# Optimization experiments

Hardware: AMD Instinct MI355X
Metric: run time of the kernel (lower is better)

## Reference

```python
import jax, jax.numpy as jnp
import numpy as np

B, N, F_, CI, C, CO = 2, 1024, 2048, 3, 80, 128
NB = 15          # DirResNet blocks
Q = C // 4


def _graph_bn(x, g, b, eps=1e-5):
    # BatchNorm over channels with stats over (batch, nodes) -- training-mode batch stats
    mu = jnp.mean(x, axis=(0, 1), keepdims=True)
    var = jnp.var(x, axis=(0, 1), keepdims=True)
    return (x - mu) * jax.lax.rsqrt(var + eps) * g + b


def _graph_conv(L, x, W0, W1, bias):
    # GraphConv with k=1: linear on [x, L @ x]
    return x @ W0 + jnp.einsum('bnm,bmc->bnc', L, x) @ W1 + bias


def _forward(inputs, L, Di, DiA, mask,
             conv1_W0, conv1_W1, conv1_b,
             rn_bn0_g, rn_bn0_b, rn_fc0_W, rn_fc0_b,
             rn_bn1_g, rn_bn1_b, rn_fc1_W, rn_fc1_b,
             bn1_g, bn1_b, bn2_g, bn2_b, bn3_g, bn3_b,
             conv2_W0, conv2_W1, conv2_b):
    v = _graph_conv(L, inputs, conv1_W0, conv1_W1, conv1_b)      # [B,N,C]
    f = jnp.zeros((B, F_, C), v.dtype)
    z = jnp.zeros_like(v)
    carry = (f, f, v, z, z)  # [f, tmp_f, v, tmp_v, tmp_v]

    def block(carry, p):
        f, tmp_f, v, tv0, tv1 = carry
        g0, b0, W0, c0, g1, b1, W1, c1 = p
        # Dirac: vertices -> faces (quaternion reshape: [B,N,C] -> [B,4N,C/4])
        Dv = jnp.matmul(Di, v.reshape(B, 4 * N, Q)).reshape(B, F_, C)
        x = jnp.concatenate([f, Dv], axis=-1)                    # [B,F,2C]
        f_new = jax.nn.elu(_graph_bn(x, g0, b0) @ W0 + c0) + tmp_f
        # Adjoint Dirac: faces -> vertices
        Df = jnp.matmul(DiA, f_new.reshape(B, 4 * F_, Q)).reshape(B, N, C)
        y = jnp.concatenate([v, Df], axis=-1)                    # [B,N,2C]
        v_new = jax.nn.elu(_graph_bn(y, g1, b1) @ W1 + c1) + tv0
        return (f_new, f, v_new, v, tv0), None

    carry, _ = jax.lax.scan(
        block, carry,
        (rn_bn0_g, rn_bn0_b, rn_fc0_W, rn_fc0_b,
         rn_bn1_g, rn_bn1_b, rn_fc1_W, rn_fc1_b))
    _, _, v2, v1, v0 = carry
    v = jax.nn.elu(_graph_bn(v2, bn1_g, bn1_b)
                   + _graph_bn(v1, bn2_g, bn2_b)
                   + _graph_bn(v0, bn3_g, bn3_b))
    # Dropout2d: identity (eval mode / deterministic reference)
    v = _graph_conv(L, v, conv2_W0, conv2_W1, conv2_b)           # [B,N,CO]
    out = (v * mask).sum(axis=1) / mask.sum(axis=1)              # masked mean pool -> [B,CO]
    return out


def setup_inputs() -> dict:
    key = jax.random.key(0)
    ks = jax.random.split(key, 32)
    s = 0.05
    d = {
        'inputs': jax.random.normal(ks[0], (B, N, CI), jnp.float32),
        'L': jax.random.normal(ks[1], (B, N, N), jnp.float32) / np.float32(np.sqrt(N)),
        'Di': jax.random.normal(ks[2], (B, 4 * F_, 4 * N), jnp.float32) / np.float32(np.sqrt(4 * N)),
        'DiA': jax.random.normal(ks[3], (B, 4 * N, 4 * F_), jnp.float32) / np.float32(np.sqrt(4 * F_)),
        'mask': (jax.random.uniform(ks[4], (B, N, 1)) > 0.2).astype(jnp.float32),
        'conv1_W0': jax.random.normal(ks[5], (CI, C), jnp.float32) * s,
        'conv1_W1': jax.random.normal(ks[6], (CI, C), jnp.float32) * s,
        'conv1_b': jax.random.normal(ks[7], (C,), jnp.float32) * s,
        'rn_bn0_g': 1.0 + 0.1 * jax.random.normal(ks[8], (NB, 2 * C), jnp.float32),
        'rn_bn0_b': s * jax.random.normal(ks[9], (NB, 2 * C), jnp.float32),
        'rn_fc0_W': jax.random.normal(ks[10], (NB, 2 * C, C), jnp.float32) * s,
        'rn_fc0_b': jax.random.normal(ks[11], (NB, C), jnp.float32) * s,
        'rn_bn1_g': 1.0 + 0.1 * jax.random.normal(ks[12], (NB, 2 * C), jnp.float32),
        'rn_bn1_b': s * jax.random.normal(ks[13], (NB, 2 * C), jnp.float32),
        'rn_fc1_W': jax.random.normal(ks[14], (NB, 2 * C, C), jnp.float32) * s,
        'rn_fc1_b': jax.random.normal(ks[15], (NB, C), jnp.float32) * s,
        'bn1_g': 1.0 + 0.1 * jax.random.normal(ks[16], (C,), jnp.float32),
        'bn1_b': s * jax.random.normal(ks[17], (C,), jnp.float32),
        'bn2_g': 1.0 + 0.1 * jax.random.normal(ks[18], (C,), jnp.float32),
        'bn2_b': s * jax.random.normal(ks[19], (C,), jnp.float32),
        'bn3_g': 1.0 + 0.1 * jax.random.normal(ks[20], (C,), jnp.float32),
        'bn3_b': s * jax.random.normal(ks[21], (C,), jnp.float32),
        'conv2_W0': jax.random.normal(ks[22], (C, CO), jnp.float32) * s,
        'conv2_W1': jax.random.normal(ks[23], (C, CO), jnp.float32) * s,
        'conv2_b': jax.random.normal(ks[24], (CO,), jnp.float32) * s,
    }
    return d


def reference(inputs, L, Di, DiA, mask,
              conv1_W0, conv1_W1, conv1_b,
              rn_bn0_g, rn_bn0_b, rn_fc0_W, rn_fc0_b,
              rn_bn1_g, rn_bn1_b, rn_fc1_W, rn_fc1_b,
              bn1_g, bn1_b, bn2_g, bn2_b, bn3_g, bn3_b,
              conv2_W0, conv2_W1, conv2_b):
    return _forward(inputs, L, Di, DiA, mask,
                    conv1_W0, conv1_W1, conv1_b,
                    rn_bn0_g, rn_bn0_b, rn_fc0_W, rn_fc0_b,
                    rn_bn1_g, rn_bn1_b, rn_fc1_W, rn_fc1_b,
                    bn1_g, bn1_b, bn2_g, bn2_b, bn3_g, bn3_b,
                    conv2_W0, conv2_W1, conv2_b)
```

## Files before the change

kernel.cpp:

```cpp
#include <hip/hip_runtime.h>
#include <cstdint>

#define BB 2
#define NN 1024
#define FF 2048
#define CC 80
#define C2 160
#define NB_ 15
#define ROWS_X (BB*FF)
#define ROWS_Y (BB*NN)
#define WTP 168

typedef __attribute__((ext_vector_type(8))) _Float16 half8;
typedef __attribute__((ext_vector_type(4))) _Float16 half4;
typedef __attribute__((ext_vector_type(4))) float f32x4;

__global__ __launch_bounds__(256) void k_conv1(
    const float* __restrict__ inp, const float* __restrict__ L,
    const float* __restrict__ W0, const float* __restrict__ W1,
    const float* __restrict__ bias, float* __restrict__ v,
    float4* __restrict__ vstat)
{
  int bx = blockIdx.x;
  int b = bx >> 6, rb = bx & 63;
  int row0 = rb * 16;
  __shared__ float red[256][3];
  __shared__ float lx[16][3];
  __shared__ float st[16][2][CC];
  int t = threadIdx.x;
  int rloc = t >> 4, sl = t & 15;
  const float* Lrow = L + ((size_t)b*NN + row0 + rloc) * NN;
  const float* ipb  = inp + (size_t)b*NN*3;
  float a0=0.f,a1=0.f,a2=0.f;
  for (int m = sl; m < NN; m += 16) {
    float lv = Lrow[m];
    a0 = fmaf(lv, ipb[m*3+0], a0);
    a1 = fmaf(lv, ipb[m*3+1], a1);
    a2 = fmaf(lv, ipb[m*3+2], a2);
  }
  red[t][0]=a0; red[t][1]=a1; red[t][2]=a2;
  __syncthreads();
  if (t < 48) {
    int row = t/3, ci = t%3;
    float s=0.f;
    for (int s2=0; s2<16; ++s2) s += red[row*16+s2][ci];
    lx[row][ci]=s;
  }
  __syncthreads();
  for (int o = t; o < 16*CC; o += 256) {
    int row = o/CC, c = o%CC;
    const float* ir = inp + ((size_t)b*NN + row0 + row)*3;
    float val = bias[c];
    #pragma unroll
    for (int ci=0; ci<3; ++ci)
      val += ir[ci]*W0[ci*CC+c] + lx[row][ci]*W1[ci*CC+c];
    v[((size_t)b*NN + row0 + row)*CC + c] = val;
    st[row][0][c] = val;
    st[row][1][c] = val*val;
  }
  __syncthreads();
  if (t < 40) {
    float s0=0.f,q0=0.f,s1=0.f,q1=0.f;
    for (int row=0; row<16; ++row){
      s0+=st[row][0][2*t];   q0+=st[row][1][2*t];
      s1+=st[row][0][2*t+1]; q1+=st[row][1][2*t+1];
    }
    vstat[(size_t)bx*40 + t] = make_float4(s0,q0,s1,q1);
  }
}

__device__ __forceinline__ unsigned pkh(float a, float b){
  _Float16 ha = (_Float16)a, hb = (_Float16)b;
  unsigned short ua = __builtin_bit_cast(unsigned short, ha);
  unsigned short ub = __builtin_bit_cast(unsigned short, hb);
  return (unsigned)ua | ((unsigned)ub << 16);
}
__global__ __launch_bounds__(256) void k_cvt(
    const float* __restrict__ src, uint4* __restrict__ dst, size_t n8)
{
  size_t i = (size_t)blockIdx.x*256 + threadIdx.x;
  size_t stride = (size_t)gridDim.x*256;
  for (; i < n8; i += stride) {
    const float4* s = (const float4*)src + i*2;
    float4 f0 = s[0], f1 = s[1];
    uint4 o;
    o.x = pkh(f0.x,f0.y); o.y = pkh(f0.z,f0.w);
    o.z = pkh(f1.x,f1.y); o.w = pkh(f1.z,f1.w);
    dst[i] = o;
  }
}

__global__ __launch_bounds__(256) __attribute__((amdgpu_waves_per_eu(2,2)))
void k_dirac_mfma(
    const _Float16* __restrict__ A, const float* __restrict__ x,
    float* __restrict__ y, float4* __restrict__ stat, int M, int K)
{
  int b = blockIdx.y;
  A += (size_t)b*M*K; x += (size_t)b*(size_t)K*20; y += (size_t)b*(size_t)M*20;
  __shared__ _Float16 xT[2][2][32][264];
  __shared__ float cb_[2][8][64];
  __shared__ float stS[2][CC], stQ[2][CC];
  int t = threadIdx.x, lane = t & 63, w = t >> 6;
  int rw = w & 1, kh = w >> 1;
  int row0 = blockIdx.x*32 + rw*16;
  int cl = lane & 15, cg = lane >> 4;
  int KH = K >> 1;
  f32x4 acc0 = {0.f,0.f,0.f,0.f}, acc1 = {0.f,0.f,0.f,0.f};
  const float4* xv = (const float4*)x;
  int nchunk = KH >> 8;
  const _Float16* Abase = A + (size_t)(row0 + cl)*K + (size_t)kh*KH + cg*8;

  for (int i = t; i < 2*2*12*264; i += 256) {
    int bb = i / (2*12*264);
    int rem = i - bb*(2*12*264);
    int hh = rem / (12*264);
    int r2 = rem - hh*(12*264);
    xT[bb][hh][20 + r2/264][r2 % 264] = (_Float16)0.f;
  }
  {
    float4 s0[5], s1[5];
    #pragma unroll
    for (int i=0;i<5;++i){ s0[i]=xv[(size_t)t*5+i]; s1[i]=xv[((size_t)KH+t)*5+i]; }
    #pragma unroll
    for (int i=0;i<5;++i){
      xT[0][0][4*i+0][t]=(_Float16)s0[i].x; xT[0][0][4*i+1][t]=(_Float16)s0[i].y;
      xT[0][0][4*i+2][t]=(_Float16)s0[i].z; xT[0][0][4*i+3][t]=(_Float16)s0[i].w;
      xT[0][1][4*i+0][t]=(_Float16)s1[i].x; xT[0][1][4*i+1][t]=(_Float16)s1[i].y;
      xT[0][1][4*i+2][t]=(_Float16)s1[i].z; xT[0][1][4*i+3][t]=(_Float16)s1[i].w;
    }
  }
  half8 a_cur[8];
  #pragma unroll
  for (int ks=0;ks<8;++ks) a_cur[ks] = *(const half8*)(Abase + ks*32);
  __syncthreads();

  for (int c=0; c<nchunk; ++c) {
    int cur = c & 1;
    bool more = (c+1 < nchunk);
    float4 s0[5], s1[5];
    half8 a_nxt[8];
    if (more) {
      size_t k0 = (size_t)(c+1)*256 + t;
      #pragma unroll
      for (int i=0;i<5;++i){ s0[i]=xv[k0*5+i]; s1[i]=xv[(k0+KH)*5+i]; }
      const _Float16* An = Abase + (size_t)(c+1)*256;
      #pragma unroll
      for (int ks=0;ks<8;++ks) a_nxt[ks] = *(const half8*)(An + ks*32);
    }
    #pragma unroll
    for (int ks=0;ks<8;++ks) {
      half8 b0 = *(const half8*)(&xT[cur][kh][cl     ][ks*32 + cg*8]);
      half8 b1 = *(const half8*)(&xT[cur][kh][16 + cl][ks*32 + cg*8]);
      acc0 = __builtin_amdgcn_mfma_f32_16x16x32_f16(a_cur[ks], b0, acc0, 0,0,0);
      acc1 = __builtin_amdgcn_mfma_f32_16x16x32_f16(a_cur[ks], b1, acc1, 0,0,0);
    }
    if (more) {
      #pragma unroll
      for (int i=0;i<5;++i){
        xT[cur^1][0][4*i+0][t]=(_Float16)s0[i].x; xT[cur^1][0][4*i+1][t]=(_Float16)s0[i].y;
        xT[cur^1][0][4*i+2][t]=(_Float16)s0[i].z; xT[cur^1][0][4*i+3][t]=(_Float16)s0[i].w;
        xT[cur^1][1][4*i+0][t]=(_Float16)s1[i].x; xT[cur^1][1][4*i+1][t]=(_Float16)s1[i].y;
        xT[cur^1][1][4*i+2][t]=(_Float16)s1[i].z; xT[cur^1][1][4*i+3][t]=(_Float16)s1[i].w;
      }
      #pragma unroll
      for (int ks=0;ks<8;++ks) a_cur[ks] = a_nxt[ks];
    }
    __syncthreads();
  }

  if (kh == 1) {
    #pragma unroll
    for (int j=0;j<4;++j){ cb_[rw][j][lane]=acc0[j]; cb_[rw][4+j][lane]=acc1[j]; }
  }
  __syncthreads();
  if (kh == 0) {
    #pragma unroll
    for (int j=0;j<4;++j){ acc0[j]+=cb_[rw][j][lane]; acc1[j]+=cb_[rw][4+j][lane]; }
    #pragma unroll
    for (int j=0;j<4;++j) {
      float v = acc0[j];
      y[(size_t)(row0 + 4*cg + j)*20 + cl] = v;
      float s = v, sq = v*v;
      s  += __shfl_xor(s,16);  s  += __shfl_xor(s,32);
      sq += __shfl_xor(sq,16); sq += __shfl_xor(sq,32);
      if (cg==0) { stS[rw][j*20+cl]=s; stQ[rw][j*20+cl]=sq; }
    }
    #pragma unroll
    for (int j=0;j<4;++j) {
      float v = acc1[j];
      if (cl < 4) y[(size_t)(row0 + 4*cg + j)*20 + 16 + cl] = v;
      float s = v, sq = v*v;
      s  += __shfl_xor(s,16);  s  += __shfl_xor(s,32);
      sq += __shfl_xor(sq,16); sq += __shfl_xor(sq,32);
      if (cg==0 && cl<4) { stS[rw][j*20+16+cl]=s; stQ[rw][j*20+16+cl]=sq; }
    }
  }
  __syncthreads();
  int slot = blockIdx.y*gridDim.x + blockIdx.x;
  if (t < 40) {
    float4 o;
    o.x = stS[0][2*t]  +stS[1][2*t];
    o.y = stQ[0][2*t]  +stQ[1][2*t];
    o.z = stS[0][2*t+1]+stS[1][2*t+1];
    o.w = stQ[0][2*t+1]+stQ[1][2*t+1];
    stat[(size_t)slot*40 + t] = o;
  }
}

__global__ __launch_bounds__(256) __attribute__((amdgpu_waves_per_eu(2,2)))
void k_dirac_f32(
    const float* __restrict__ A, const float* __restrict__ x,
    float* __restrict__ y, float4* __restrict__ stat, int M, int K)
{
  const int DR = 4;
  int b = blockIdx.y;
  A += (size_t)b*M*K; x += (size_t)b*(size_t)K*20; y += (size_t)b*(size_t)M*20;
  __shared__ float xs[2][20][256];
  __shared__ float stS[4][CC], stQ[4][CC];
  int t = threadIdx.x, lane = t & 63, w = t >> 6;
  int row0 = blockIdx.x*(4*DR) + w*DR;
  float acc[DR][20];
  #pragma unroll
  for (int r=0;r<DR;++r)
    #pragma unroll
    for (int q=0;q<20;++q) acc[r][q]=0.f;
  const float4* xv = (const float4*)x;
  int nchunk = K >> 8;
  const float* Abase = A + (size_t)row0*K + (lane<<2);
  {
    float4 s0[5];
    #pragma unroll
    for (int i=0;i<5;++i) s0[i] = xv[(size_t)t*5 + i];
    #pragma unroll
    for (int i=0;i<5;++i) {
      xs[0][4*i+0][t]=s0[i].x; xs[0][4*i+1][t]=s0[i].y;
      xs[0][4*i+2][t]=s0[i].z; xs[0][4*i+3][t]=s0[i].w;
    }
  }
  float4 a[DR];
  #pragma unroll
  for (int r=0;r<DR;++r) a[r] = *(const float4*)(Abase + (size_t)r*K);
  __syncthreads();
  for (int c=0; c<nchunk; ++c) {
    int cur = c & 1;
    bool more = (c+1 < nchunk);
    float4 st[5];
    if (more) {
      size_t kb = (size_t)(c+1)*256 + t;
      #pragma unroll
      for (int i=0;i<5;++i) st[i] = xv[kb*5 + i];
    }
    float4 af[DR];
    #pragma unroll
    for (int r=0;r<DR;++r) af[r] = a[r];
    if (more) {
      const float* An = Abase + (size_t)(c+1)*256;
      #pragma unroll
      for (int r=0;r<DR;++r) a[r] = *(const float4*)(An + (size_t)r*K);
    }
    #pragma unroll
    for (int q=0;q<20;++q) {
      float4 xq = *(const float4*)(&xs[cur][q][lane<<2]);
      #pragma unroll
      for (int r=0;r<DR;++r) {
        acc[r][q] = fmaf(af[r].x, xq.x, acc[r][q]);
        acc[r][q] = fmaf(af[r].y, xq.y, acc[r][q]);
        acc[r][q] = fmaf(af[r].z, xq.z, acc[r][q]);
        acc[r][q] = fmaf(af[r].w, xq.w, acc[r][q]);
      }
    }
    if (more) {
      #pragma unroll
      for (int i=0;i<5;++i) {
        xs[cur^1][4*i+0][t]=st[i].x; xs[cur^1][4*i+1][t]=st[i].y;
        xs[cur^1][4*i+2][t]=st[i].z; xs[cur^1][4*i+3][t]=st[i].w;
      }
    }
    __syncthreads();
  }
  #pragma unroll
  for (int r=0;r<DR;++r) {
    #pragma unroll
    for (int q=0;q<20;++q) {
      float s = acc[r][q];
      s += __shfl_xor(s, 1);  s += __shfl_xor(s, 2);
      s += __shfl_xor(s, 4);  s += __shfl_xor(s, 8);
      s += __shfl_xor(s, 16); s += __shfl_xor(s, 32);
      acc[r][q]=s;
    }
    if (lane==0) {
      float4* yp = (float4*)(y + (size_t)(row0+r)*20);
      yp[0] = make_float4(acc[r][0],acc[r][1],acc[r][2],acc[r][3]);
      yp[1] = make_float4(acc[r][4],acc[r][5],acc[r][6],acc[r][7]);
      yp[2] = make_float4(acc[r][8],acc[r][9],acc[r][10],acc[r][11]);
      yp[3] = make_float4(acc[r][12],acc[r][13],acc[r][14],acc[r][15]);
      yp[4] = make_float4(acc[r][16],acc[r][17],acc[r][18],acc[r][19]);
    }
  }
  if (lane == 0) {
    #pragma unroll
    for (int r=0;r<DR;++r)
      #pragma unroll
      for (int q=0;q<20;++q) {
        float v0 = acc[r][q];
        stS[w][r*20+q] = v0;
        stQ[w][r*20+q] = v0*v0;
      }
  }
  __syncthreads();
  int slot = blockIdx.y*gridDim.x + blockIdx.x;
  if (t < 40) {
    float4 o;
    o.x = stS[0][2*t]+stS[1][2*t]+stS[2][2*t]+stS[3][2*t];
    o.y = stQ[0][2*t]+stQ[1][2*t]+stQ[2][2*t]+stQ[3][2*t];
    o.z = stS[0][2*t+1]+stS[1][2*t+1]+stS[2][2*t+1]+stS[3][2*t+1];
    o.w = stQ[0][2*t+1]+stQ[1][2*t+1]+stQ[2][2*t+1]+stQ[3][2*t+1];
    stat[(size_t)slot*40 + t] = o;
  }
}

__global__ __launch_bounds__(320) void k_fc(
    const float* __restrict__ p1, const float* __restrict__ p2,
    const float4* __restrict__ sp1, int ns1,
    const float4* __restrict__ sp2, int ns2,
    const float* __restrict__ g, const float* __restrict__ bb,
    const float* __restrict__ W, const float* __restrict__ cb,
    const float* add, float* out,
    float4* __restrict__ statout, int rows, float invrows)
{
  __shared__ _Float16 Wt[80*WTP];
  __shared__ _Float16 xh[16*WTP];
  __shared__ float ad[2][C2];
  __shared__ float bpl[CC];
  __shared__ float4 pst[2][2][40];
  __shared__ float stS[CC], stQ[CC];
  int t = threadIdx.x;
  int lane = t & 63, wv = t >> 6;
  int cl = lane & 15, cg = lane >> 4;
  int r0 = blockIdx.x * 16;

  if (t < 160) {
    int p = t % 40, s = (t/40) & 1, h = t/80;
    const float4* sp = s ? sp2 : sp1;
    int ns = s ? ns2 : ns1;
    int half = ns >> 1;
    const float4* base = sp + (size_t)(h*half)*40 + p;
    float4 acc = {0.f,0.f,0.f,0.f};
    int i=0;
    for (; i+8<=half; i+=8) {
      float4 v[8];
      #pragma unroll
      for (int j=0;j<8;++j) v[j] = base[(size_t)(i+j)*40];
      #pragma unroll
      for (int j=0;j<8;++j){ acc.x+=v[j].x; acc.y+=v[j].y; acc.z+=v[j].z; acc.w+=v[j].w; }
    }
    for (; i<half; ++i){
      float4 v = base[(size_t)i*40];
      acc.x+=v.x; acc.y+=v.y; acc.z+=v.z; acc.w+=v.w;
    }
    pst[h][s][p] = acc;
  } else {
    int t2 = t - 160;
    #pragma unroll
    for (int i=0;i<20;++i) {
      int f4 = t2 + i*160;
      float4 w4 = ((const float4*)W)[f4];
      int c2 = f4/20, c = (f4%20)*4;
      Wt[(c+0)*WTP + c2] = (_Float16)w4.x;
      Wt[(c+1)*WTP + c2] = (_Float16)w4.y;
      Wt[(c+2)*WTP + c2] = (_Float16)w4.z;
      Wt[(c+3)*WTP + c2] = (_Float16)w4.w;
    }
  }
  __syncthreads();

  half8 bfr[5];
  #pragma unroll
  for (int ks=0;ks<5;++ks)
    bfr[ks] = *(const half8*)(&Wt[(wv*16+cl)*WTP + ks*32 + cg*8]);
  if (t < C2) {
    int s = (t < CC) ? 0 : 1;
    int chl = (t < CC) ? t : t - CC;
    int p = chl >> 1, e = chl & 1;
    float4 a0 = pst[0][s][p], a1 = pst[1][s][p];
    float S = e ? (a0.z + a1.z) : (a0.x + a1.x);
    float Q = e ? (a0.w + a1.w) : (a0.y + a1.y);
    float mean = S*invrows;
    float var  = fmaf(-mean, mean, Q*invrows);
    float aa   = g[t]*rsqrtf(var + 1e-5f);
    ad[0][t]=aa; ad[1][t]= bb[t] - mean*aa;
  }
  __syncthreads();

  #pragma unroll
  for (int i=0;i<2;++i) {
    int f4 = t + i*320;
    if (f4 < 640) {
      int row = f4/40, cq = (f4%40)*4;
      const float* src = (cq < 80) ? (p1 + (size_t)(r0+row)*CC + cq)
                                   : (p2 + (size_t)(r0+row)*CC + cq - 80);
      float4 x4 = *(const float4*)src;
      half4 h4;
      h4[0]=(_Float16)(x4.x*ad[0][cq+0]); h4[1]=(_Float16)(x4.y*ad[0][cq+1]);
      h4[2]=(_Float16)(x4.z*ad[0][cq+2]); h4[3]=(_Float16)(x4.w*ad[0][cq+3]);
      *(half4*)(&xh[row*WTP + cq]) = h4;
    }
  }
  if (t < CC) {
    float s = cb[t];
    #pragma unroll
    for (int ks=0;ks<20;++ks) {
      half8 w8 = *(const half8*)(&Wt[t*WTP + ks*8]);
      #pragma unroll
      for (int j=0;j<8;++j) s = fmaf(ad[1][ks*8+j], (float)w8[j], s);
    }
    bpl[t]=s;
  }
  __syncthreads();

  half8 afr[5];
  #pragma unroll
  for (int ks=0;ks<5;++ks)
    afr[ks] = *(const half8*)(&xh[cl*WTP + ks*32 + cg*8]);
  f32x4 acc = {0.f,0.f,0.f,0.f};
  #pragma unroll
  for (int ks=0;ks<5;++ks)
    acc = __builtin_amdgcn_mfma_f32_16x16x32_f16(afr[ks], bfr[ks], acc, 0,0,0);
  float ss=0.f, sq=0.f;
  int col = wv*16 + cl;
  #pragma unroll
  for (int j=0;j<4;++j) {
    int row = r0 + 4*cg + j;
    float val = acc[j] + bpl[col];
    val = val>0.f ? val : expm1f(val);
    val += add[(size_t)row*CC + col];
    out[(size_t)row*CC + col] = val;
    ss += val; sq = fmaf(val,val,sq);
  }
  ss += __shfl_xor(ss,16); ss += __shfl_xor(ss,32);
  sq += __shfl_xor(sq,16); sq += __shfl_xor(sq,32);
  if (cg==0) { stS[col]=ss; stQ[col]=sq; }
  __syncthreads();
  if (t < 40)
    statout[(size_t)blockIdx.x*40 + t] = make_float4(stS[2*t], stQ[2*t], stS[2*t+1], stQ[2*t+1]);
}

__global__ __launch_bounds__(256) void k_final(
    const float* __restrict__ v2, const float* __restrict__ v1, const float* __restrict__ v0,
    const float4* __restrict__ s2, const float4* __restrict__ s1, const float4* __restrict__ s0,
    const float* __restrict__ g1, const float* __restrict__ b1,
    const float* __restrict__ g2, const float* __restrict__ b2,
    const float* __restrict__ g3, const float* __restrict__ b3,
    float* __restrict__ vf, int ns)
{
  __shared__ float A[3][CC], D[3][CC];
  __shared__ float4 pf[2][3][40];
  int t = threadIdx.x;
  if (t < 240) {
    int p = t % 40, s = (t/40) % 3, h = t/120;
    const float4* sp = s==0 ? s2 : (s==1 ? s1 : s0);
    int half = ns >> 1;
    const float4* base = sp + (size_t)(h*half)*40 + p;
    float4 acc = {0.f,0.f,0.f,0.f};
    int i=0;
    for (; i+8<=half; i+=8) {
      float4 v[8];
      #pragma unroll
      for (int j=0;j<8;++j) v[j] = base[(size_t)(i+j)*40];
      #pragma unroll
      for (int j=0;j<8;++j){ acc.x+=v[j].x; acc.y+=v[j].y; acc.z+=v[j].z; acc.w+=v[j].w; }
    }
    for (; i<half; ++i){
      float4 v = base[(size_t)i*40];
      acc.x+=v.x; acc.y+=v.y; acc.z+=v.z; acc.w+=v.w;
    }
    pf[h][s][p] = acc;
  }
  __syncthreads();
  if (t < 240) {
    int set = t/80, chl = t%80, p = chl>>1, e = chl&1;
    const float* gg  = set==0? g1 : (set==1? g2 : g3);
    const float* bbp = set==0? b1 : (set==1? b2 : b3);
    float4 a0 = pf[0][set][p], a1 = pf[1][set][p];
    float S = e ? (a0.z + a1.z) : (a0.x + a1.x);
    float Q = e ? (a0.w + a1.w) : (a0.y + a1.y);
    float mean = S*(1.f/ROWS_Y);
    float var  = fmaf(-mean,mean,Q*(1.f/ROWS_Y));
    float aa   = gg[chl]*rsqrtf(var+1e-5f);
    A[set][chl]=aa; D[set][chl]=bbp[chl]-mean*aa;
  }
  __syncthreads();
  for (size_t idx = (size_t)blockIdx.x*256 + t; idx < (size_t)ROWS_Y*CC; idx += (size_t)gridDim.x*256) {
    int c = (int)(idx % CC);
    float val = fmaf(v2[idx],A[0][c],D[0][c]) + fmaf(v1[idx],A[1][c],D[1][c]) + fmaf(v0[idx],A[2][c],D[2][c]);
    vf[idx] = val>0.f? val : expm1f(val);
  }
}

__global__ __launch_bounds__(256) void k_w(
    const float* __restrict__ mask, const float* __restrict__ L, float* __restrict__ w)
{
  int bx = blockIdx.x;
  int b = bx >> 4, n0 = (bx & 15) * 64;
  int t = threadIdx.x;
  int ks = t >> 6;
  __shared__ float red[4][64];
  float acc=0.f;
  const float* Lb = L + (size_t)b*NN*NN;
  const float* mb = mask + b*NN;
  int n = n0 + (t & 63);
  for (int k = ks*256; k < ks*256+256; k+=8) {
    float mv[8], lv[8];
    #pragma unroll
    for (int j=0;j<8;++j){ mv[j]=mb[k+j]; lv[j]=Lb[(size_t)(k+j)*NN + n]; }
    #pragma unroll
    for (int j=0;j<8;++j) acc = fmaf(mv[j], lv[j], acc);
  }
  red[ks][t&63]=acc;
  __syncthreads();
  if (t < 64) w[b*NN + n0 + t] = red[0][t]+red[1][t]+red[2][t]+red[3][t];
}

__global__ __launch_bounds__(256) void k_pool(
    const float* __restrict__ vf, const float* __restrict__ mask,
    const float* __restrict__ w, float* __restrict__ part)
{
  int bx = blockIdx.x;
  int b = bx >> 3, slab = bx & 7;
  int t = threadIdx.x, c = t%CC, rs = t/CC;
  __shared__ float st[3][2][CC];
  if (t<240) {
    float a1=0.f,a2=0.f;
    for (int r = rs; r < 128; r += 3) {
      int row = slab*128 + r;
      float val = vf[((size_t)b*NN + row)*CC + c];
      a1 = fmaf(mask[b*NN+row], val, a1);
      a2 = fmaf(w[b*NN+row],    val, a2);
    }
    st[rs][0][c]=a1; st[rs][1][c]=a2;
  }
  __syncthreads();
  if (t<CC) {
    part[((b*8+slab)*2+0)*CC+t] = st[0][0][t]+st[1][0][t]+st[2][0][t];
    part[((b*8+slab)*2+1)*CC+t] = st[0][1][t]+st[1][1][t]+st[2][1][t];
  }
}

__global__ __launch_bounds__(256) void k_out(
    const float* __restrict__ part, const float* __restrict__ mask,
    const float* __restrict__ W0, const float* __restrict__ W1,
    const float* __restrict__ b2, float* __restrict__ outp)
{
  __shared__ float pl[2][2][CC];
  __shared__ float msred[2][128];
  __shared__ float ms[2];
  int t = threadIdx.x;
  {
    int b = t >> 7, k0 = t & 127;
    float m[8];
    #pragma unroll
    for (int j=0;j<8;++j) m[j] = mask[b*NN + k0 + j*128];
    msred[b][k0] = ((m[0]+m[1])+(m[2]+m[3]))+((m[4]+m[5])+(m[6]+m[7]));
  }
  if (t < 160) {
    int b = t/CC, c = t%CC;
    float v1[8], v2[8];
    #pragma unroll
    for (int slab=0; slab<8; ++slab){
      v1[slab] = part[((b*8+slab)*2+0)*CC+c];
      v2[slab] = part[((b*8+slab)*2+1)*CC+c];
    }
    float s1=0.f,s2=0.f;
    #pragma unroll
    for (int slab=0;slab<8;++slab){ s1+=v1[slab]; s2+=v2[slab]; }
    pl[b][0][c]=s1; pl[b][1][c]=s2;
  }
  __syncthreads();
  if (t < 2) {
    float s=0.f;
    for (int k=0;k<128;++k) s += msred[t][k];
    ms[t]=s;
  }
  __syncthreads();
  int b = t >> 7, co = t & 127;
  float acc = 0.f;
  for (int c=0;c<CC;c+=8) {
    float w0[8], w1[8];
    #pragma unroll
    for (int j=0;j<8;++j){ w0[j]=W0[(c+j)*128+co]; w1[j]=W1[(c+j)*128+co]; }
    #pragma unroll
    for (int j=0;j<8;++j) acc += pl[b][0][c+j]*w0[j] + pl[b][1][c+j]*w1[j];
  }
  outp[t] = acc/ms[b] + b2[co];
}

extern "C" void kernel_launch(void* const* d_in, const int* in_sizes, int n_in,
                              void* d_out, int out_size, void* d_ws, size_t ws_size,
                              hipStream_t stream)
{
  const float* inp  = (const float*)d_in[0];
  const float* L    = (const float*)d_in[1];
  const float* Di   = (const float*)d_in[2];
  const float* DiA  = (const float*)d_in[3];
  const float* mask = (const float*)d_in[4];
  const float* c1W0 = (const float*)d_in[5];
  const float* c1W1 = (const float*)d_in[6];
  const float* c1b  = (const float*)d_in[7];
  const float* bn0g = (const float*)d_in[8];
  const float* bn0b = (const float*)d_in[9];
  const float* fc0W = (const float*)d_in[10];
  const float* fc0b = (const float*)d_in[11];
  const float* bn1g = (const float*)d_in[12];
  const float* bn1b = (const float*)d_in[13];
  const float* fc1W = (const float*)d_in[14];
  const float* fc1b = (const float*)d_in[15];
  const float* fbn1g= (const float*)d_in[16];
  const float* fbn1b= (const float*)d_in[17];
  const float* fbn2g= (const float*)d_in[18];
  const float* fbn2b= (const float*)d_in[19];
  const float* fbn3g= (const float*)d_in[20];
  const float* fbn3b= (const float*)d_in[21];
  const float* c2W0 = (const float*)d_in[22];
  const float* c2W1 = (const float*)d_in[23];
  const float* c2b  = (const float*)d_in[24];

  float* ws = (float*)d_ws;
  size_t off = 0;
  auto alloc = [&](size_t n)->float* { float* p = ws + off; off += (n + 63) & ~(size_t)63; return p; };
  const size_t STFL = (size_t)1024*40*4;
  float* vb[3];   for (int i=0;i<3;++i) vb[i]   = alloc((size_t)BB*NN*CC);
  float* fb[2];   for (int i=0;i<2;++i) fb[i]   = alloc((size_t)BB*FF*CC);
  float* Dv       = alloc((size_t)BB*FF*CC);
  float* Df       = alloc((size_t)BB*NN*CC);
  float4* vstat[3];for (int i=0;i<3;++i) vstat[i]= (float4*)alloc(STFL);
  float4* fstat[2];for (int i=0;i<2;++i) fstat[i]= (float4*)alloc(STFL);
  float4* dvstat  = (float4*)alloc(STFL);
  float4* dfstat  = (float4*)alloc(STFL);
  float* vf       = alloc((size_t)BB*NN*CC);
  float* wv       = alloc((size_t)BB*NN);
  float* part     = alloc((size_t)16*2*CC);
  const size_t nDi = (size_t)BB*(4*FF)*(4*NN);
  _Float16* Dih  = (_Float16*)alloc(nDi/2);
  _Float16* DiAh = (_Float16*)alloc(nDi/2);
  bool usebf = (off*sizeof(float) <= ws_size);

  hipMemsetAsync(fb[0],    0, (size_t)BB*FF*CC*4, stream);
  hipMemsetAsync(fb[1],    0, (size_t)BB*FF*CC*4, stream);
  hipMemsetAsync(vb[1],    0, (size_t)BB*NN*CC*4, stream);
  hipMemsetAsync(fstat[0], 0, (size_t)256*40*16, stream);

  if (usebf) {
    k_cvt<<<4096,256,0,stream>>>(Di,  (uint4*)Dih,  nDi/8);
    k_cvt<<<4096,256,0,stream>>>(DiA, (uint4*)DiAh, nDi/8);
  }

  k_conv1<<<128,256,0,stream>>>(inp, L, c1W0, c1W1, c1b, vb[0], vstat[0]);

  int nsDv = usebf ? 512 : 1024;
  int nsDf = usebf ? 256 : 512;
  int cur=0, p1=1, p2=2, fcur=0, fs=0;
  for (int it=0; it<NB_; ++it) {
    if (usebf) k_dirac_mfma<<<dim3(256,2),256,0,stream>>>(Dih, vb[cur], Dv, dvstat, 4*FF, 4*NN);
    else       k_dirac_f32 <<<dim3(512,2),256,0,stream>>>(Di,  vb[cur], Dv, dvstat, 4*FF, 4*NN);
    k_fc<<<ROWS_X/16,320,0,stream>>>(fb[fcur], Dv, fstat[fs],256, dvstat,nsDv,
        bn0g+(size_t)it*C2, bn0b+(size_t)it*C2, fc0W+(size_t)it*C2*CC, fc0b+(size_t)it*CC,
        fb[1-fcur], fb[1-fcur], fstat[1-fs], ROWS_X, 1.f/ROWS_X);
    fcur = 1-fcur; fs = 1-fs;
    if (usebf) k_dirac_mfma<<<dim3(128,2),256,0,stream>>>(DiAh, fb[fcur], Df, dfstat, 4*NN, 4*FF);
    else       k_dirac_f32 <<<dim3(256,2),256,0,stream>>>(DiA,  fb[fcur], Df, dfstat, 4*NN, 4*FF);
    k_fc<<<ROWS_Y/16,320,0,stream>>>(vb[cur], Df, vstat[cur],128, dfstat,nsDf,
        bn1g+(size_t)it*C2, bn1b+(size_t)it*C2, fc1W+(size_t)it*C2*CC, fc1b+(size_t)it*CC,
        vb[p1], vb[p2], vstat[p2], ROWS_Y, 1.f/ROWS_Y);
    int tmp=p2; p2=p1; p1=cur; cur=tmp;
  }

  k_final<<<128,256,0,stream>>>(vb[cur],vb[p1],vb[p2], vstat[cur],vstat[p1],vstat[p2],
      fbn1g,fbn1b,fbn2g,fbn2b,fbn3g,fbn3b, vf, 128);
  k_w<<<32,256,0,stream>>>(mask, L, wv);
  k_pool<<<16,256,0,stream>>>(vf, mask, wv, part);
  k_out<<<1,256,0,stream>>>(part, mask, c2W0, c2W1, c2b, (float*)d_out);
}
```

Before: 1.957 ms.

## Fuse fp16 Dirac conversion into first matmul and emit transposed fp16 activations from producers

```diff
diff --git a/kernel.cpp b/kernel.cpp
--- a/kernel.cpp
+++ b/kernel.cpp
@@ -19,7 +19,7 @@
     const float* __restrict__ inp, const float* __restrict__ L,
     const float* __restrict__ W0, const float* __restrict__ W1,
     const float* __restrict__ bias, float* __restrict__ v,
-    float4* __restrict__ vstat)
+    float4* __restrict__ vstat, _Float16* __restrict__ vT)
 {
   int bx = blockIdx.x;
   int b = bx >> 6, rb = bx & 63;
@@ -55,6 +55,7 @@
     for (int ci=0; ci<3; ++ci)
       val += ir[ci]*W0[ci*CC+c] + lx[row][ci]*W1[ci*CC+c];
     v[((size_t)b*NN + row0 + row)*CC + c] = val;
+    vT[((size_t)b*32 + c%20)*(4*NN) + (row0+row)*4 + c/20] = (_Float16)val;
     st[row][0][c] = val;
     st[row][1][c] = val*val;
   }
@@ -69,113 +70,91 @@
   }
 }
 
-__device__ __forceinline__ unsigned pkh(float a, float b){
-  _Float16 ha = (_Float16)a, hb = (_Float16)b;
-  unsigned short ua = __builtin_bit_cast(unsigned short, ha);
-  unsigned short ub = __builtin_bit_cast(unsigned short, hb);
-  return (unsigned)ua | ((unsigned)ub << 16);
-}
-__global__ __launch_bounds__(256) void k_cvt(
-    const float* __restrict__ src, uint4* __restrict__ dst, size_t n8)
-{
-  size_t i = (size_t)blockIdx.x*256 + threadIdx.x;
-  size_t stride = (size_t)gridDim.x*256;
-  for (; i < n8; i += stride) {
-    const float4* s = (const float4*)src + i*2;
-    float4 f0 = s[0], f1 = s[1];
-    uint4 o;
-    o.x = pkh(f0.x,f0.y); o.y = pkh(f0.z,f0.w);
-    o.z = pkh(f1.x,f1.y); o.w = pkh(f1.z,f1.w);
-    dst[i] = o;
-  }
-}
-
+template<int KSPLIT, bool CVT>
 __global__ __launch_bounds__(256) __attribute__((amdgpu_waves_per_eu(2,2)))
-void k_dirac_mfma(
-    const _Float16* __restrict__ A, const float* __restrict__ x,
+void k_dirac2(
+    const void* __restrict__ Ain, _Float16* __restrict__ Aout,
+    const _Float16* __restrict__ xTg,
     float* __restrict__ y, float4* __restrict__ stat, int M, int K)
 {
+  constexpr int RT = 4/KSPLIT;
   int b = blockIdx.y;
-  A += (size_t)b*M*K; x += (size_t)b*(size_t)K*20; y += (size_t)b*(size_t)M*20;
-  __shared__ _Float16 xT[2][2][32][264];
-  __shared__ float cb_[2][8][64];
-  __shared__ float stS[2][CC], stQ[2][CC];
+  const _Float16* Ah = (const _Float16*)Ain + (size_t)b*M*K;
+  const float*    Af = (const float*)Ain    + (size_t)b*M*K;
+  _Float16* Ao = Aout + (size_t)b*M*K;
+  const _Float16* xTb = xTg + (size_t)b*32*K;
+  y += (size_t)b*(size_t)M*20;
+  __shared__ float cb_[4][8][64];
+  __shared__ float stS[RT][CC], stQ[RT][CC];
   int t = threadIdx.x, lane = t & 63, w = t >> 6;
-  int rw = w & 1, kh = w >> 1;
-  int row0 = blockIdx.x*32 + rw*16;
+  int rw = (RT==2) ? (w & 1) : 0;
+  int kh = (RT==2) ? (w >> 1) : w;
+  int row0 = blockIdx.x*(16*RT) + rw*16;
   int cl = lane & 15, cg = lane >> 4;
-  int KH = K >> 1;
+  int KW = K / KSPLIT;
+  const int NS = KW >> 5;
+  int kbase = kh*KW;
   f32x4 acc0 = {0.f,0.f,0.f,0.f}, acc1 = {0.f,0.f,0.f,0.f};
-  const float4* xv = (const float4*)x;
-  int nchunk = KH >> 8;
-  const _Float16* Abase = A + (size_t)(row0 + cl)*K + (size_t)kh*KH + cg*8;
-
-  for (int i = t; i < 2*2*12*264; i += 256) {
-    int bb = i / (2*12*264);
-    int rem = i - bb*(2*12*264);
-    int hh = rem / (12*264);
-    int r2 = rem - hh*(12*264);
-    xT[bb][hh][20 + r2/264][r2 % 264] = (_Float16)0.f;
-  }
-  {
-    float4 s0[5], s1[5];
-    #pragma unroll
-    for (int i=0;i<5;++i){ s0[i]=xv[(size_t)t*5+i]; s1[i]=xv[((size_t)KH+t)*5+i]; }
-    #pragma unroll
-    for (int i=0;i<5;++i){
-      xT[0][0][4*i+0][t]=(_Float16)s0[i].x; xT[0][0][4*i+1][t]=(_Float16)s0[i].y;
-      xT[0][0][4*i+2][t]=(_Float16)s0[i].z; xT[0][0][4*i+3][t]=(_Float16)s0[i].w;
-      xT[0][1][4*i+0][t]=(_Float16)s1[i].x; xT[0][1][4*i+1][t]=(_Float16)s1[i].y;
-      xT[0][1][4*i+2][t]=(_Float16)s1[i].z; xT[0][1][4*i+3][t]=(_Float16)s1[i].w;
-    }
-  }
-  half8 a_cur[8];
-  #pragma unroll
-  for (int ks=0;ks<8;++ks) a_cur[ks] = *(const half8*)(Abase + ks*32);
-  __syncthreads();
-
-  for (int c=0; c<nchunk; ++c) {
-    int cur = c & 1;
-    bool more = (c+1 < nchunk);
-    float4 s0[5], s1[5];
-    half8 a_nxt[8];
-    if (more) {
-      size_t k0 = (size_t)(c+1)*256 + t;
-      #pragma unroll
-      for (int i=0;i<5;++i){ s0[i]=xv[k0*5+i]; s1[i]=xv[(k0+KH)*5+i]; }
-      const _Float16* An = Abase + (size_t)(c+1)*256;
-      #pragma unroll
-      for (int ks=0;ks<8;++ks) a_nxt[ks] = *(const half8*)(An + ks*32);
-    }
-    #pragma unroll
-    for (int ks=0;ks<8;++ks) {
-      half8 b0 = *(const half8*)(&xT[cur][kh][cl     ][ks*32 + cg*8]);
-      half8 b1 = *(const half8*)(&xT[cur][kh][16 + cl][ks*32 + cg*8]);
-      acc0 = __builtin_amdgcn_mfma_f32_16x16x32_f16(a_cur[ks], b0, acc0, 0,0,0);
-      acc1 = __builtin_amdgcn_mfma_f32_16x16x32_f16(a_cur[ks], b1, acc1, 0,0,0);
-    }
-    if (more) {
-      #pragma unroll
-      for (int i=0;i<5;++i){
-        xT[cur^1][0][4*i+0][t]=(_Float16)s0[i].x; xT[cur^1][0][4*i+1][t]=(_Float16)s0[i].y;
-        xT[cur^1][0][4*i+2][t]=(_Float16)s0[i].z; xT[cur^1][0][4*i+3][t]=(_Float16)s0[i].w;
-        xT[cur^1][1][4*i+0][t]=(_Float16)s1[i].x; xT[cur^1][1][4*i+1][t]=(_Float16)s1[i].y;
-        xT[cur^1][1][4*i+2][t]=(_Float16)s1[i].z; xT[cur^1][1][4*i+3][t]=(_Float16)s1[i].w;
+  size_t aoff = (size_t)(row0 + cl)*K + kbase + cg*8;
+  const _Float16* xb0 = xTb + (size_t)cl*K      + kbase + cg*8;
+  const _Float16* xb1 = xTb + (size_t)(16+cl)*K + kbase + cg*8;
+
+  auto MF = [&](half8 a, int s) {
+    half8 b0 = *(const half8*)(xb0 + (size_t)s*32);
+    half8 b1 = *(const half8*)(xb1 + (size_t)s*32);
+    acc0 = __builtin_amdgcn_mfma_f32_16x16x32_f16(a, b0, acc0, 0,0,0);
+    acc1 = __builtin_amdgcn_mfma_f32_16x16x32_f16(a, b1, acc1, 0,0,0);
+  };
+
+  if constexpr (!CVT) {
+    auto ldh = [&](int s)->half8 { return *(const half8*)(Ah + aoff + (size_t)s*32); };
+    half8 A0=ldh(0), A1=ldh(1), A2=ldh(2), A3=ldh(3);
+    int s = 0;
+    for (; s < NS-4; s += 4) {
+      MF(A0, s  ); A0 = ldh(s+4);
+      MF(A1, s+1); A1 = ldh(s+5);
+      MF(A2, s+2); A2 = ldh(s+6);
+      MF(A3, s+3); A3 = ldh(s+7);
+    }
+    MF(A0, s); MF(A1, s+1); MF(A2, s+2); MF(A3, s+3);
+  } else {
+    auto ldf = [&](int s, float4& xa, float4& xb){
+      const float* p = Af + aoff + (size_t)s*32;
+      xa = *(const float4*)p; xb = *(const float4*)(p+4);
+    };
+    auto CMF = [&](float4 fa, float4 fb, int s) {
+      half8 a;
+      a[0]=(_Float16)fa.x; a[1]=(_Float16)fa.y; a[2]=(_Float16)fa.z; a[3]=(_Float16)fa.w;
+      a[4]=(_Float16)fb.x; a[5]=(_Float16)fb.y; a[6]=(_Float16)fb.z; a[7]=(_Float16)fb.w;
+      *(half8*)(Ao + aoff + (size_t)s*32) = a;
+      MF(a, s);
+    };
+    float4 F0a,F0b,F1a,F1b,F2a,F2b,F3a,F3b;
+    ldf(0,F0a,F0b); ldf(1,F1a,F1b); ldf(2,F2a,F2b); ldf(3,F3a,F3b);
+    int s = 0;
+    for (; s < NS-4; s += 4) {
+      CMF(F0a,F0b,s  ); ldf(s+4,F0a,F0b);
+      CMF(F1a,F1b,s+1); ldf(s+5,F1a,F1b);
+      CMF(F2a,F2b,s+2); ldf(s+6,F2a,F2b);
+      CMF(F3a,F3b,s+3); ldf(s+7,F3a,F3b);
+    }
+    CMF(F0a,F0b,s); CMF(F1a,F1b,s+1); CMF(F2a,F2b,s+2); CMF(F3a,F3b,s+3);
+  }
+
+  if (w >= RT) {
+    #pragma unroll
+    for (int j=0;j<4;++j){ cb_[w][j][lane]=acc0[j]; cb_[w][4+j][lane]=acc1[j]; }
+  }
+  __syncthreads();
+  if (kh == 0) {
+    #pragma unroll
+    for (int q=1;q<KSPLIT;++q) {
+      #pragma unroll
+      for (int j=0;j<4;++j){
+        acc0[j] += cb_[q*RT+rw][j][lane];
+        acc1[j] += cb_[q*RT+rw][4+j][lane];
       }
-      #pragma unroll
-      for (int ks=0;ks<8;++ks) a_cur[ks] = a_nxt[ks];
-    }
-    __syncthreads();
-  }
-
-  if (kh == 1) {
-    #pragma unroll
-    for (int j=0;j<4;++j){ cb_[rw][j][lane]=acc0[j]; cb_[rw][4+j][lane]=acc1[j]; }
-  }
-  __syncthreads();
-  if (kh == 0) {
-    #pragma unroll
-    for (int j=0;j<4;++j){ acc0[j]+=cb_[rw][j][lane]; acc1[j]+=cb_[rw][4+j][lane]; }
+    }
     #pragma unroll
     for (int j=0;j<4;++j) {
       float v = acc0[j];
@@ -198,11 +177,12 @@
   __syncthreads();
   int slot = blockIdx.y*gridDim.x + blockIdx.x;
   if (t < 40) {
-    float4 o;
-    o.x = stS[0][2*t]  +stS[1][2*t];
-    o.y = stQ[0][2*t]  +stQ[1][2*t];
-    o.z = stS[0][2*t+1]+stS[1][2*t+1];
-    o.w = stQ[0][2*t+1]+stQ[1][2*t+1];
+    float4 o = {0.f,0.f,0.f,0.f};
+    #pragma unroll
+    for (int r=0;r<RT;++r){
+      o.x += stS[r][2*t];   o.y += stQ[r][2*t];
+      o.z += stS[r][2*t+1]; o.w += stQ[r][2*t+1];
+    }
     stat[(size_t)slot*40 + t] = o;
   }
 }
@@ -326,7 +306,8 @@
     const float* __restrict__ g, const float* __restrict__ bb,
     const float* __restrict__ W, const float* __restrict__ cb,
     const float* add, float* out,
-    float4* __restrict__ statout, int rows, float invrows)
+    float4* __restrict__ statout, int rows, float invrows,
+    _Float16* __restrict__ xTout, int rpbs)
 {
   __shared__ _Float16 Wt[80*WTP];
   __shared__ _Float16 xh[16*WTP];
@@ -428,6 +409,9 @@
     acc = __builtin_amdgcn_mfma_f32_16x16x32_f16(afr[ks], bfr[ks], acc, 0,0,0);
   float ss=0.f, sq=0.f;
   int col = wv*16 + cl;
+  int q20 = col % 20, c4 = col / 20;
+  size_t Kx = (size_t)4 << rpbs;
+  int rpbm = (1 << rpbs) - 1;
   #pragma unroll
   for (int j=0;j<4;++j) {
     int row = r0 + 4*cg + j;
@@ -435,6 +419,9 @@
     val = val>0.f ? val : expm1f(val);
     val += add[(size_t)row*CC + col];
     out[(size_t)row*CC + col] = val;
+    int bb2 = row >> rpbs;
+    int kx = ((row & rpbm) << 2) + c4;
+    xTout[((size_t)bb2*32 + q20)*Kx + kx] = (_Float16)val;
     ss += val; sq = fmaf(val,val,sq);
   }
   ss += __shfl_xor(ss,16); ss += __shfl_xor(ss,32);
@@ -639,6 +626,8 @@
   float* vf       = alloc((size_t)BB*NN*CC);
   float* wv       = alloc((size_t)BB*NN);
   float* part     = alloc((size_t)16*2*CC);
+  _Float16* xTv   = (_Float16*)alloc((size_t)BB*32*(4*NN)/2);
+  _Float16* xTf   = (_Float16*)alloc((size_t)BB*32*(4*FF)/2);
   const size_t nDi = (size_t)BB*(4*FF)*(4*NN);
   _Float16* Dih  = (_Float16*)alloc(nDi/2);
   _Float16* DiAh = (_Float16*)alloc(nDi/2);
@@ -649,28 +638,31 @@
   hipMemsetAsync(vb[1],    0, (size_t)BB*NN*CC*4, stream);
   hipMemsetAsync(fstat[0], 0, (size_t)256*40*16, stream);
 
-  if (usebf) {
-    k_cvt<<<4096,256,0,stream>>>(Di,  (uint4*)Dih,  nDi/8);
-    k_cvt<<<4096,256,0,stream>>>(DiA, (uint4*)DiAh, nDi/8);
-  }
-
-  k_conv1<<<128,256,0,stream>>>(inp, L, c1W0, c1W1, c1b, vb[0], vstat[0]);
+  k_conv1<<<128,256,0,stream>>>(inp, L, c1W0, c1W1, c1b, vb[0], vstat[0], xTv);
 
   int nsDv = usebf ? 512 : 1024;
-  int nsDf = usebf ? 256 : 512;
+  int nsDf = usebf ? 512 : 512;
   int cur=0, p1=1, p2=2, fcur=0, fs=0;
   for (int it=0; it<NB_; ++it) {
-    if (usebf) k_dirac_mfma<<<dim3(256,2),256,0,stream>>>(Dih, vb[cur], Dv, dvstat, 4*FF, 4*NN);
-    else       k_dirac_f32 <<<dim3(512,2),256,0,stream>>>(Di,  vb[cur], Dv, dvstat, 4*FF, 4*NN);
+    if (usebf) {
+      if (it==0) k_dirac2<2,true ><<<dim3(256,2),256,0,stream>>>(Di,  Dih, xTv, Dv, dvstat, 4*FF, 4*NN);
+      else       k_dirac2<2,false><<<dim3(256,2),256,0,stream>>>(Dih, Dih, xTv, Dv, dvstat, 4*FF, 4*NN);
+    } else {
+      k_dirac_f32<<<dim3(512,2),256,0,stream>>>(Di, vb[cur], Dv, dvstat, 4*FF, 4*NN);
+    }
     k_fc<<<ROWS_X/16,320,0,stream>>>(fb[fcur], Dv, fstat[fs],256, dvstat,nsDv,
         bn0g+(size_t)it*C2, bn0b+(size_t)it*C2, fc0W+(size_t)it*C2*CC, fc0b+(size_t)it*CC,
-        fb[1-fcur], fb[1-fcur], fstat[1-fs], ROWS_X, 1.f/ROWS_X);
+        fb[1-fcur], fb[1-fcur], fstat[1-fs], ROWS_X, 1.f/ROWS_X, xTf, 11);
     fcur = 1-fcur; fs = 1-fs;
-    if (usebf) k_dirac_mfma<<<dim3(128,2),256,0,stream>>>(DiAh, fb[fcur], Df, dfstat, 4*NN, 4*FF);
-    else       k_dirac_f32 <<<dim3(256,2),256,0,stream>>>(DiA,  fb[fcur], Df, dfstat, 4*NN, 4*FF);
+    if (usebf) {
+      if (it==0) k_dirac2<4,true ><<<dim3(256,2),256,0,stream>>>(DiA,  DiAh, xTf, Df, dfstat, 4*NN, 4*FF);
+      else       k_dirac2<4,false><<<dim3(256,2),256,0,stream>>>(DiAh, DiAh, xTf, Df, dfstat, 4*NN, 4*FF);
+    } else {
+      k_dirac_f32<<<dim3(256,2),256,0,stream>>>(DiA, fb[fcur], Df, dfstat, 4*NN, 4*FF);
+    }
     k_fc<<<ROWS_Y/16,320,0,stream>>>(vb[cur], Df, vstat[cur],128, dfstat,nsDf,
         bn1g+(size_t)it*C2, bn1b+(size_t)it*C2, fc1W+(size_t)it*C2*CC, fc1b+(size_t)it*CC,
-        vb[p1], vb[p2], vstat[p2], ROWS_Y, 1.f/ROWS_Y);
+        vb[p1], vb[p2], vstat[p2], ROWS_Y, 1.f/ROWS_Y, xTv, 10);
     int tmp=p2; p2=p1; p1=cur; cur=tmp;
   }
 
```

New measurement: 2.308 ms. +17.9%, slower.
